# Performance work log

Measured on AMD Instinct MI355X. Metric: run time of the kernel, lower is better.

Reference implementation:

```python
import jax, jax.numpy as jnp
import numpy as np

B, S, D = 2, 2048, 2048
H, DH, DC = 16, 128, 32  # heads, head dim, compressed dim


def setup_inputs() -> dict:
    key = jax.random.key(0)
    ks = jax.random.split(key, 9)
    sc = 0.02
    return {
        "hidden_states": jax.random.normal(ks[0], (B, S, D), jnp.float32),
        "Wq": jax.random.normal(ks[1], (D, D), jnp.float32) * sc,
        "Wk": jax.random.normal(ks[2], (D, D), jnp.float32) * sc,
        "Wv": jax.random.normal(ks[3], (D, D), jnp.float32) * sc,
        "Wo": jax.random.normal(ks[4], (D, D), jnp.float32) * sc,
        "Wkc": jax.random.normal(ks[5], (DH, DC), jnp.float32) * sc,
        "Wvc": jax.random.normal(ks[6], (DH, DC), jnp.float32) * sc,
        "Wke": jax.random.normal(ks[7], (DC, DH), jnp.float32) * sc,
        "Wve": jax.random.normal(ks[8], (DC, DH), jnp.float32) * sc,
    }


def reference(hidden_states, Wq, Wk, Wv, Wo, Wkc, Wvc, Wke, Wve):
    # Project to per-head Q/K/V: [B, H, S, DH]
    def proj(W):
        return jnp.einsum("bsd,de->bse", hidden_states, W).reshape(B, S, H, DH).transpose(0, 2, 1, 3)

    q = proj(Wq)
    k_full = proj(Wk)
    v_full = proj(Wv)

    # Compress K/V (low-rank down-projection, per head): [B, H, S, DC]
    k_compressed = jnp.einsum("bhsd,dc->bhsc", k_full, Wkc)
    v_compressed = jnp.einsum("bhsd,dc->bhsc", v_full, Wvc)

    # Expand compressed cache back to full head dim (expand_mode='pre')
    k_hat = jnp.einsum("bhsc,cd->bhsd", k_compressed, Wke)
    v_hat = jnp.einsum("bhsc,cd->bhsd", v_compressed, Wve)

    # Causal scaled-dot-product attention
    scale = 1.0 / jnp.sqrt(jnp.asarray(DH, jnp.float32))
    scores = jnp.einsum("bhqd,bhkd->bhqk", q, k_hat) * scale
    causal = jnp.tril(jnp.ones((S, S), bool))
    scores = jnp.where(causal[None, None], scores, jnp.finfo(scores.dtype).min)
    probs = jax.nn.softmax(scores, axis=-1)
    ctx = jnp.einsum("bhqk,bhkd->bhqd", probs, v_hat)  # [B, H, S, DH]

    attn_out = jnp.einsum("bsd,de->bse", ctx.transpose(0, 2, 1, 3).reshape(B, S, D), Wo)
    return attn_out, k_compressed, v_compressed
```

## Files before the change

kernel.cpp:

```cpp
#include <hip/hip_runtime.h>

using u16 = unsigned short;
using u32 = unsigned int;

typedef __attribute__((ext_vector_type(8))) __bf16 bf16x8;
typedef __attribute__((ext_vector_type(4))) float f32x4;
typedef __attribute__((ext_vector_type(4))) u32 u32x4;

#define GLOAD16(gp, lp) __builtin_amdgcn_global_load_lds( \
    (const __attribute__((address_space(1))) void*)(gp),  \
    (__attribute__((address_space(3))) void*)(lp), 16, 0, 0)

__device__ __forceinline__ u16 f2b(float f) {
  u32 u = __builtin_bit_cast(u32, f);
  u += 0x7fffu + ((u >> 16) & 1u);
  return (u16)(u >> 16);
}
__device__ __forceinline__ float b2f(u16 h) {
  return __builtin_bit_cast(float, (u32)h << 16);
}

__global__ __launch_bounds__(256) void cast_k(
    const float* __restrict__ in, u16* __restrict__ o1, int n) {
  int i = (blockIdx.x * 256 + threadIdx.x) * 4;
  if (i >= n) return;
  float4 v = *(const float4*)&in[i];
  *(uint2*)&o1[i] = make_uint2((u32)f2b(v.x) | ((u32)f2b(v.y) << 16),
                               (u32)f2b(v.z) | ((u32)f2b(v.w) << 16));
}

__global__ __launch_bounds__(256) void transpose_cast_k(
    const float* __restrict__ in, u16* __restrict__ out, int D) {
  __shared__ float t[32][33];
  const int tx = threadIdx.x & 31, ty = threadIdx.x >> 5;
  const int e0 = blockIdx.x * 32, d0 = blockIdx.y * 32;
  #pragma unroll
  for (int i = ty; i < 32; i += 8) t[i][tx] = in[(size_t)(d0 + i) * D + e0 + tx];
  __syncthreads();
  #pragma unroll
  for (int i = ty; i < 32; i += 8) out[(size_t)(e0 + i) * D + d0 + tx] = f2b(t[tx][i]);
}

__global__ __launch_bounds__(256) void combine_k(
    const float* __restrict__ Wfull, const float* __restrict__ Wc,
    u16* __restrict__ outT, int D) {
  __shared__ float wl[4096];
  const int tid = threadIdx.x;
  for (int i = tid; i < 4096; i += 256) wl[i] = Wc[i];
  __syncthreads();
  const int h = blockIdx.y;
  const int d = blockIdx.x * 256 + tid;
  const float* wkr = Wfull + (size_t)d * D + h * 128;
  float acc[32] = {};
  for (int dp = 0; dp < 128; ++dp) {
    const float wv = wkr[dp];
    const float* w2 = &wl[dp * 32];
    #pragma unroll
    for (int c = 0; c < 32; ++c) acc[c] += wv * w2[c];
  }
  #pragma unroll
  for (int c = 0; c < 32; ++c)
    outT[(size_t)(h * 32 + c) * D + d] = f2b(acc[c]);
}

__global__ __launch_bounds__(256) void wtrans_k(
    const float* __restrict__ in, u16* __restrict__ out) {
  const int i = blockIdx.x * 256 + threadIdx.x;
  const int d = i >> 5, c = i & 31;
  out[i] = f2b(in[c * 128 + d]);
}

template <int TRANS>
__global__ __launch_bounds__(256) void expand_mfma_k(
    const u16* __restrict__ in, const u16* __restrict__ WT, u16* __restrict__ out) {
  __shared__ alignas(16) u16 WL[128 * 32];
  __shared__ alignas(16) u16 ct[64 * 40];
  const int tid = threadIdx.x, lane = tid & 63, w = tid >> 6;
  const int cl = lane & 15, g = lane >> 4;
  const int bh = blockIdx.y, s0 = blockIdx.x * 64;
  for (int i = tid; i < 512; i += 256) ((uint4*)WL)[i] = ((const uint4*)WT)[i];
  {
    const int r = tid >> 2, co = (tid & 3) * 8;
    *(uint4*)&ct[r * 40 + co] =
        *(const uint4*)&in[((size_t)bh * 2048 + s0 + r) * 32 + co];
  }
  __syncthreads();
  f32x4 acc[2][4] = {};
  #pragma unroll
  for (int dti = 0; dti < 2; ++dti) {
    const bf16x8 wf = *(const bf16x8*)&WL[((w * 2 + dti) * 16 + cl) * 32 + g * 8];
    #pragma unroll
    for (int st = 0; st < 4; ++st) {
      const bf16x8 cf = *(const bf16x8*)&ct[(st * 16 + cl) * 40 + g * 8];
      if constexpr (TRANS)
        acc[dti][st] = __builtin_amdgcn_mfma_f32_16x16x32_bf16(wf, cf, acc[dti][st], 0, 0, 0);
      else
        acc[dti][st] = __builtin_amdgcn_mfma_f32_16x16x32_bf16(cf, wf, acc[dti][st], 0, 0, 0);
    }
  }
  #pragma unroll
  for (int dti = 0; dti < 2; ++dti) {
    #pragma unroll
    for (int st = 0; st < 4; ++st) {
      #pragma unroll
      for (int r = 0; r < 4; ++r) {
        if constexpr (TRANS) {
          const int d = (w * 2 + dti) * 16 + g * 4 + r;
          const int s = s0 + st * 16 + cl;
          out[((size_t)bh * 128 + d) * 2048 + s] = f2b(acc[dti][st][r]);
        } else {
          const int s = s0 + st * 16 + g * 4 + r;
          const int d = (w * 2 + dti) * 16 + cl;
          out[((size_t)bh * 2048 + s) * 128 + d] = f2b(acc[dti][st][r]);
        }
      }
    }
  }
}

__global__ __launch_bounds__(256) void gemm_qkv_k(
    const u16* __restrict__ A, const u16* __restrict__ Bt,
    u16* __restrict__ qb, float* __restrict__ out_kc, u16* __restrict__ kcb,
    float* __restrict__ out_vc, u16* __restrict__ vcb) {
  __shared__ alignas(16) u16 As[128 * 64];
  __shared__ alignas(16) u16 Bs[128 * 64];
  const int tid = threadIdx.x, lane = tid & 63, w = tid >> 6;
  const int l15 = lane & 15, lhi = lane >> 4;
  const int m0 = blockIdx.y * 128, n0 = blockIdx.x * 128;
  const int wr = (w >> 1) * 64, wc = (w & 1) * 64;
  const int rl = lane >> 3, cbe = (lane & 7) * 8;
  const int K = 2048;

  f32x4 acc[4][4] = {};

  for (int k0 = 0; k0 < K; k0 += 64) {
    __syncthreads();
    #pragma unroll
    for (int i = 0; i < 4; ++i) {
      const int rb = w * 32 + i * 8;
      GLOAD16(A + (size_t)(m0 + rb + rl) * K + k0 + cbe, &As[rb * 64]);
      GLOAD16(Bt + (size_t)(n0 + rb + rl) * K + k0 + cbe, &Bs[rb * 64]);
    }
    __syncthreads();
    #pragma unroll
    for (int ks = 0; ks < 2; ++ks) {
      bf16x8 af[4], bfr[4];
      #pragma unroll
      for (int m = 0; m < 4; ++m)
        af[m] = *(const bf16x8*)&As[(wr + m * 16 + l15) * 64 + ks * 32 + lhi * 8];
      #pragma unroll
      for (int n = 0; n < 4; ++n)
        bfr[n] = *(const bf16x8*)&Bs[(wc + n * 16 + l15) * 64 + ks * 32 + lhi * 8];
      #pragma unroll
      for (int m = 0; m < 4; ++m)
        #pragma unroll
        for (int n = 0; n < 4; ++n)
          acc[m][n] = __builtin_amdgcn_mfma_f32_16x16x32_bf16(af[m], bfr[n], acc[m][n], 0, 0, 0);
    }
  }

  const float qscale = 0.08838834764831845f;
  #pragma unroll
  for (int m = 0; m < 4; ++m) {
    #pragma unroll
    for (int n = 0; n < 4; ++n) {
      #pragma unroll
      for (int r = 0; r < 4; ++r) {
        const int row = m0 + wr + m * 16 + lhi * 4 + r;
        const int col = n0 + wc + n * 16 + l15;
        const int b = row >> 11, s = row & 2047;
        const float v = acc[m][n][r];
        if (n0 < 2048) {
          const int h = col >> 7, dh = col & 127;
          qb[((size_t)(b * 16 + h) * 2048 + s) * 128 + dh] = f2b(v * qscale);
        } else {
          const int cc = col - 2048;
          if (cc < 512) {
            const int h = cc >> 5, c = cc & 31;
            const size_t idx = ((size_t)(b * 16 + h) * 2048 + s) * 32 + c;
            out_kc[idx] = v;
            kcb[idx] = f2b(v);
          } else {
            const int cc2 = cc - 512;
            const int h = cc2 >> 5, c = cc2 & 31;
            const size_t idx = ((size_t)(b * 16 + h) * 2048 + s) * 32 + c;
            out_vc[idx] = v;
            vcb[idx] = f2b(v);
          }
        }
      }
    }
  }
}

__global__ __launch_bounds__(256) void gemm_o_k(
    const u16* __restrict__ A, const u16* __restrict__ Bt,
    int M, int N, int K, float* __restrict__ outF) {
  __shared__ alignas(16) u16 As[128 * 64];
  __shared__ alignas(16) u16 Bs[128 * 64];
  const int tid = threadIdx.x, lane = tid & 63, w = tid >> 6;
  const int l15 = lane & 15, lhi = lane >> 4;
  const int m0 = blockIdx.y * 128, n0 = blockIdx.x * 128;
  const int wr = (w >> 1) * 64, wc = (w & 1) * 64;
  const int rl = lane >> 3, cbe = (lane & 7) * 8;

  f32x4 acc[4][4] = {};

  for (int k0 = 0; k0 < K; k0 += 64) {
    __syncthreads();
    #pragma unroll
    for (int i = 0; i < 4; ++i) {
      const int rb = w * 32 + i * 8;
      GLOAD16(A + (size_t)(m0 + rb + rl) * K + k0 + cbe, &As[rb * 64]);
      GLOAD16(Bt + (size_t)(n0 + rb + rl) * K + k0 + cbe, &Bs[rb * 64]);
    }
    __syncthreads();
    #pragma unroll
    for (int ks = 0; ks < 2; ++ks) {
      bf16x8 af[4], bfr[4];
      #pragma unroll
      for (int m = 0; m < 4; ++m)
        af[m] = *(const bf16x8*)&As[(wr + m * 16 + l15) * 64 + ks * 32 + lhi * 8];
      #pragma unroll
      for (int n = 0; n < 4; ++n)
        bfr[n] = *(const bf16x8*)&Bs[(wc + n * 16 + l15) * 64 + ks * 32 + lhi * 8];
      #pragma unroll
      for (int m = 0; m < 4; ++m)
        #pragma unroll
        for (int n = 0; n < 4; ++n)
          acc[m][n] = __builtin_amdgcn_mfma_f32_16x16x32_bf16(af[m], bfr[n], acc[m][n], 0, 0, 0);
    }
  }

  #pragma unroll
  for (int m = 0; m < 4; ++m)
    #pragma unroll
    for (int n = 0; n < 4; ++n)
      #pragma unroll
      for (int r = 0; r < 4; ++r)
        outF[(size_t)(m0 + wr + m * 16 + lhi * 4 + r) * N + n0 + wc + n * 16 + l15] =
            acc[m][n][r];
}

__global__ __launch_bounds__(256) void attn_k(
    const u16* __restrict__ q, const u16* __restrict__ kh,
    const u16* __restrict__ vt, u16* __restrict__ ctx) {
  __shared__ alignas(16) u16 Ks[64 * 128];
  __shared__ alignas(16) u16 Vs[128 * 64];
  const int tid = threadIdx.x, lane = tid & 63, w = tid >> 6;
  const int c = lane & 15, g = lane >> 4;
  const int qt = blockIdx.x, bh = blockIdx.y;
  const size_t base = (size_t)bh * (2048 * 128);

  bf16x8 qf[4];
  const int qrow = qt * 64 + w * 16 + c;
  #pragma unroll
  for (int ks = 0; ks < 4; ++ks)
    qf[ks] = *(const bf16x8*)&q[base + (size_t)qrow * 128 + ks * 32 + g * 8];

  f32x4 of[8] = {};
  float m = -__builtin_inff(), l = 0.f;
  const int srcLo = lane ^ (((4 - g) & 3) << 4);
  const int srcHi = lane ^ (((g + 1) & 3) << 4);
  const int alS = (lane & 48) + ((lane & 48) >> 2);
  const bool hiSel = (g >> 1) != 0;

  for (int j = 0; j <= qt; ++j) {
    __syncthreads();
    #pragma unroll
    for (int i = 0; i < 4; ++i) {
      const int rowgrp = w * 16 + i * 4;
      const int rloc = rowgrp + (lane >> 4);
      const int srce = ((c * 16) ^ ((rloc & 7) << 4)) >> 1;
      GLOAD16(kh + base + (size_t)(j * 64 + rloc) * 128 + srce, &Ks[rowgrp * 128]);
    }
    #pragma unroll
    for (int i = 0; i < 4; ++i) {
      const int d0 = (w * 4 + i) * 8;
      const int dd = d0 + (lane >> 3);
      const int cc = lane & 7;
      GLOAD16(vt + base + (size_t)dd * 2048 + j * 64 + ((cc ^ (dd & 7)) * 8),
              &Vs[d0 * 64]);
    }
    __syncthreads();

    f32x4 sf[4] = {};
    #pragma unroll
    for (int n = 0; n < 4; ++n) {
      const int row = n * 16 + c;
      const char* kb = (const char*)Ks + row * 256;
      #pragma unroll
      for (int ks = 0; ks < 4; ++ks) {
        const bf16x8 kf = *(const bf16x8*)(kb + ((ks * 64 + g * 16) ^ ((row & 7) << 4)));
        sf[n] = __builtin_amdgcn_mfma_f32_16x16x32_bf16(kf, qf[ks], sf[n], 0, 0, 0);
      }
    }
    if (j == qt) {
      const int qloc = w * 16 + c;
      #pragma unroll
      for (int n = 0; n < 4; ++n)
        #pragma unroll
        for (int r = 0; r < 4; ++r)
          if (n * 16 + g * 4 + r > qloc) sf[n][r] = -__builtin_inff();
    }
    float smax = sf[0][0];
    #pragma unroll
    for (int n = 0; n < 4; ++n)
      #pragma unroll
      for (int r = 0; r < 4; ++r) smax = fmaxf(smax, sf[n][r]);
    smax = fmaxf(smax, __shfl_xor(smax, 16, 64));
    smax = fmaxf(smax, __shfl_xor(smax, 32, 64));
    if (__any(smax - m > 8.0f)) {
      const float mn = fmaxf(m, smax);
      const float al = __expf(m - mn);
      m = mn;
      l *= al;
      float alr[4];
      #pragma unroll
      for (int r = 0; r < 4; ++r) alr[r] = __shfl(al, alS + r, 64);
      #pragma unroll
      for (int nd = 0; nd < 8; ++nd)
        #pragma unroll
        for (int r = 0; r < 4; ++r) of[nd][r] *= alr[r];
    }
    float rs = 0.f;
    #pragma unroll
    for (int n = 0; n < 4; ++n)
      #pragma unroll
      for (int r = 0; r < 4; ++r) {
        const float p = __expf(sf[n][r] - m);
        sf[n][r] = p;
        rs += p;
      }
    rs += __shfl_xor(rs, 16, 64);
    rs += __shfl_xor(rs, 32, 64);
    l += rs;
    u32 pk0[4], pk1[4];
    #pragma unroll
    for (int n = 0; n < 4; ++n) {
      pk0[n] = (u32)f2b(sf[n][0]) | ((u32)f2b(sf[n][1]) << 16);
      pk1[n] = (u32)f2b(sf[n][2]) | ((u32)f2b(sf[n][3]) << 16);
    }
    bf16x8 pf[2];
    #pragma unroll
    for (int ks2 = 0; ks2 < 2; ++ks2) {
      const int na = ks2 * 2, nb = ks2 * 2 + 1;
      const u32 a0 = (u32)__shfl((int)pk0[na], srcLo, 64);
      const u32 b0 = (u32)__shfl((int)pk0[nb], srcLo, 64);
      const u32 a1 = (u32)__shfl((int)pk1[na], srcLo, 64);
      const u32 b1 = (u32)__shfl((int)pk1[nb], srcLo, 64);
      const u32 a2 = (u32)__shfl((int)pk0[na], srcHi, 64);
      const u32 b2 = (u32)__shfl((int)pk0[nb], srcHi, 64);
      const u32 a3 = (u32)__shfl((int)pk1[na], srcHi, 64);
      const u32 b3 = (u32)__shfl((int)pk1[nb], srcHi, 64);
      const u32x4 wv = {hiSel ? b0 : a0, hiSel ? b1 : a1, hiSel ? b2 : a2, hiSel ? b3 : a3};
      pf[ks2] = __builtin_bit_cast(bf16x8, wv);
    }
    #pragma unroll
    for (int ks2 = 0; ks2 < 2; ++ks2) {
      #pragma unroll
      for (int nd = 0; nd < 8; ++nd) {
        const int row = nd * 16 + c;
        const bf16x8 vf = *(const bf16x8*)((const char*)Vs + row * 128 +
                                           ((ks2 * 64 + g * 16) ^ ((row & 7) << 4)));
        of[nd] = __builtin_amdgcn_mfma_f32_16x16x32_bf16(pf[ks2], vf, of[nd], 0, 0, 0);
      }
    }
  }
  float linv[4];
  #pragma unroll
  for (int r = 0; r < 4; ++r) linv[r] = 1.0f / __shfl(l, alS + r, 64);
  const int bq = bh >> 4, hq = bh & 15;
  #pragma unroll
  for (int nd = 0; nd < 8; ++nd) {
    #pragma unroll
    for (int r = 0; r < 4; ++r) {
      const int row = qt * 64 + w * 16 + g * 4 + r;
      ctx[((size_t)(bq * 2048 + row)) * 2048 + hq * 128 + nd * 16 + c] =
          f2b(of[nd][r] * linv[r]);
    }
  }
}

extern "C" void kernel_launch(void* const* d_in, const int* in_sizes, int n_in,
                              void* d_out, int out_size, void* d_ws, size_t ws_size,
                              hipStream_t stream) {
  const float* hs  = (const float*)d_in[0];
  const float* Wq  = (const float*)d_in[1];
  const float* Wk  = (const float*)d_in[2];
  const float* Wv  = (const float*)d_in[3];
  const float* Wo  = (const float*)d_in[4];
  const float* Wkc = (const float*)d_in[5];
  const float* Wvc = (const float*)d_in[6];
  const float* Wke = (const float*)d_in[7];
  const float* Wve = (const float*)d_in[8];
  float* out      = (float*)d_out;
  float* out_attn = out;
  float* out_kc   = out + 8388608;
  float* out_vc   = out_kc + 2097152;

  char* ws = (char*)d_ws;
  u16* hsb   = (u16*)ws; ws += 16777216;
  u16* BtAll = (u16*)ws; ws += 12582912;
  u16* kcb   = (u16*)ws; ws += 4194304;
  u16* vcb   = (u16*)ws; ws += 4194304;
  u16* WoT   = (u16*)ws; ws += 8388608;
  u16* qb    = (u16*)ws; ws += 16777216;
  u16* vht   = (u16*)ws; ws += 16777216;
  u16* WkeT  = (u16*)ws; ws += 8192;
  u16* WveT  = (u16*)ws; ws += 8192;
  u16* khb   = hsb;
  u16* ctxb  = BtAll;

  cast_k<<<8192, 256, 0, stream>>>(hs, hsb, 8388608);
  transpose_cast_k<<<dim3(64, 64), 256, 0, stream>>>(Wq, BtAll, 2048);
  transpose_cast_k<<<dim3(64, 64), 256, 0, stream>>>(Wo, WoT, 2048);
  combine_k<<<dim3(8, 16), 256, 0, stream>>>(Wk, Wkc, BtAll + (size_t)2048 * 2048, 2048);
  combine_k<<<dim3(8, 16), 256, 0, stream>>>(Wv, Wvc, BtAll + (size_t)2560 * 2048, 2048);
  wtrans_k<<<16, 256, 0, stream>>>(Wke, WkeT);
  wtrans_k<<<16, 256, 0, stream>>>(Wve, WveT);

  gemm_qkv_k<<<dim3(24, 32), 256, 0, stream>>>(hsb, BtAll, qb, out_kc, kcb, out_vc, vcb);

  expand_mfma_k<0><<<dim3(32, 32), 256, 0, stream>>>(kcb, WkeT, khb);
  expand_mfma_k<1><<<dim3(32, 32), 256, 0, stream>>>(vcb, WveT, vht);

  attn_k<<<dim3(32, 32), 256, 0, stream>>>(qb, khb, vht, ctxb);

  gemm_o_k<<<dim3(16, 32), 256, 0, stream>>>(ctxb, WoT, 4096, 2048, 2048, out_attn);
}
```

Before: 494.9 us.

## Pair causal query tiles per block, double-buffer K/V, use exp2 softmax

Each attention block now handles two query tiles (i and 31-i), so every block does the same amount of causal work and the K/V tiles loaded for the longer tile are reused by the shorter one. K/V staging is double-buffered so the next tile's global-to-LDS loads overlap compute, cutting one barrier per iteration. The log2(e) factor is folded into the Q scale so softmax can use exp2f, P is packed to bf16 with the hardware cvt_pk instruction, and the rescale threshold is raised. In exchange the grid is halved to 512 blocks, register and LDS use per block grow, which may lower occupancy.

```diff
diff --git a/kernel.cpp b/kernel.cpp
--- a/kernel.cpp
+++ b/kernel.cpp
@@ -18,6 +18,11 @@
 }
 __device__ __forceinline__ float b2f(u16 h) {
   return __builtin_bit_cast(float, (u32)h << 16);
+}
+__device__ __forceinline__ u32 cvtpk(float lo, float hi) {
+  u32 r;
+  asm("v_cvt_pk_bf16_f32 %0, %1, %2" : "=v"(r) : "v"(lo), "v"(hi));
+  return r;
 }
 
 __global__ __launch_bounds__(256) void cast_k(
@@ -159,7 +164,7 @@
     }
   }
 
-  const float qscale = 0.08838834764831845f;
+  const float qscale = 0.08838834764831845f * 1.4426950408889634f;
   #pragma unroll
   for (int m = 0; m < 4; ++m) {
     #pragma unroll
@@ -245,141 +250,185 @@
 __global__ __launch_bounds__(256) void attn_k(
     const u16* __restrict__ q, const u16* __restrict__ kh,
     const u16* __restrict__ vt, u16* __restrict__ ctx) {
-  __shared__ alignas(16) u16 Ks[64 * 128];
-  __shared__ alignas(16) u16 Vs[128 * 64];
+  __shared__ alignas(16) u16 Ks[2][64 * 128];
+  __shared__ alignas(16) u16 Vs[2][128 * 64];
   const int tid = threadIdx.x, lane = tid & 63, w = tid >> 6;
   const int c = lane & 15, g = lane >> 4;
-  const int qt = blockIdx.x, bh = blockIdx.y;
+  const int iA = blockIdx.x, iB = 31 - iA, bh = blockIdx.y;
   const size_t base = (size_t)bh * (2048 * 128);
 
-  bf16x8 qf[4];
-  const int qrow = qt * 64 + w * 16 + c;
-  #pragma unroll
-  for (int ks = 0; ks < 4; ++ks)
-    qf[ks] = *(const bf16x8*)&q[base + (size_t)qrow * 128 + ks * 32 + g * 8];
-
-  f32x4 of[8] = {};
-  float m = -__builtin_inff(), l = 0.f;
+  bf16x8 qfA[4], qfB[4];
+  {
+    const int qrA = iA * 64 + w * 16 + c;
+    const int qrB = iB * 64 + w * 16 + c;
+    #pragma unroll
+    for (int ks = 0; ks < 4; ++ks) {
+      qfA[ks] = *(const bf16x8*)&q[base + (size_t)qrA * 128 + ks * 32 + g * 8];
+      qfB[ks] = *(const bf16x8*)&q[base + (size_t)qrB * 128 + ks * 32 + g * 8];
+    }
+  }
+
+  f32x4 ofA[8] = {}, ofB[8] = {};
+  float mA = -__builtin_inff(), lA = 0.f;
+  float mB = -__builtin_inff(), lB = 0.f;
   const int srcLo = lane ^ (((4 - g) & 3) << 4);
   const int srcHi = lane ^ (((g + 1) & 3) << 4);
   const int alS = (lane & 48) + ((lane & 48) >> 2);
   const bool hiSel = (g >> 1) != 0;
 
-  for (int j = 0; j <= qt; ++j) {
+#define STAGE(J, BUF)                                                          \
+  {                                                                            \
+    _Pragma("unroll")                                                          \
+    for (int i2 = 0; i2 < 4; ++i2) {                                           \
+      const int rowgrp = w * 16 + i2 * 4;                                      \
+      const int rloc = rowgrp + (lane >> 4);                                   \
+      const int srce = ((c * 16) ^ ((rloc & 7) << 4)) >> 1;                    \
+      GLOAD16(kh + base + (size_t)((J) * 64 + rloc) * 128 + srce,              \
+              &Ks[BUF][rowgrp * 128]);                                         \
+    }                                                                          \
+    _Pragma("unroll")                                                          \
+    for (int i2 = 0; i2 < 4; ++i2) {                                           \
+      const int d0 = (w * 4 + i2) * 8;                                         \
+      const int dd = d0 + (lane >> 3);                                         \
+      const int cc = lane & 7;                                                 \
+      GLOAD16(vt + base + (size_t)dd * 2048 + (J) * 64 + ((cc ^ (dd & 7)) * 8),\
+              &Vs[BUF][d0 * 64]);                                              \
+    }                                                                          \
+  }
+
+#define DO_GROUP(QF, OF, MM, LL, QTILE, J, BUF)                                \
+  {                                                                            \
+    f32x4 sf[4] = {};                                                          \
+    const char* ksb0 = (const char*)&Ks[BUF][0];                               \
+    _Pragma("unroll")                                                          \
+    for (int n = 0; n < 4; ++n) {                                              \
+      const int row = n * 16 + c;                                              \
+      const char* kb = ksb0 + row * 256;                                       \
+      _Pragma("unroll")                                                        \
+      for (int ks = 0; ks < 4; ++ks) {                                         \
+        const bf16x8 kf =                                                      \
+            *(const bf16x8*)(kb + ((ks * 64 + g * 16) ^ ((row & 7) << 4)));    \
+        sf[n] = __builtin_amdgcn_mfma_f32_16x16x32_bf16(kf, QF[ks], sf[n],     \
+                                                        0, 0, 0);              \
+      }                                                                        \
+    }                                                                          \
+    if ((J) == (QTILE)) {                                                      \
+      const int qloc = w * 16 + c;                                             \
+      _Pragma("unroll")                                                        \
+      for (int n = 0; n < 4; ++n)                                              \
+        _Pragma("unroll")                                                      \
+        for (int r = 0; r < 4; ++r)                                            \
+          if (n * 16 + g * 4 + r > qloc) sf[n][r] = -__builtin_inff();         \
+    }                                                                          \
+    float smax = sf[0][0];                                                     \
+    _Pragma("unroll")                                                          \
+    for (int n = 0; n < 4; ++n)                                                \
+      _Pragma("unroll")                                                        \
+      for (int r = 0; r < 4; ++r) smax = fmaxf(smax, sf[n][r]);                \
+    smax = fmaxf(smax, __shfl_xor(smax, 16, 64));                              \
+    smax = fmaxf(smax, __shfl_xor(smax, 32, 64));                              \
+    if (__any(smax - (MM) > 12.0f)) {                                          \
+      const float mn = fmaxf(MM, smax);                                        \
+      const float al = exp2f((MM) - mn);                                       \
+      MM = mn;                                                                 \
+      LL *= al;                                                                \
+      float alr[4];                                                            \
+      _Pragma("unroll")                                                        \
+      for (int r = 0; r < 4; ++r) alr[r] = __shfl(al, alS + r, 64);            \
+      _Pragma("unroll")                                                        \
+      for (int nd = 0; nd < 8; ++nd)                                           \
+        _Pragma("unroll")                                                      \
+        for (int r = 0; r < 4; ++r) OF[nd][r] *= alr[r];                       \
+    }                                                                          \
+    float rs = 0.f;                                                            \
+    _Pragma("unroll")                                                          \
+    for (int n = 0; n < 4; ++n)                                                \
+      _Pragma("unroll")                                                        \
+      for (int r = 0; r < 4; ++r) {                                            \
+        const float p = exp2f(sf[n][r] - (MM));                                \
+        sf[n][r] = p;                                                          \
+        rs += p;                                                               \
+      }                                                                        \
+    rs += __shfl_xor(rs, 16, 64);                                              \
+    rs += __shfl_xor(rs, 32, 64);                                              \
+    LL += rs;                                                                  \
+    u32 pk0[4], pk1[4];                                                        \
+    _Pragma("unroll")                                                          \
+    for (int n = 0; n < 4; ++n) {                                              \
+      pk0[n] = cvtpk(sf[n][0], sf[n][1]);                                      \
+      pk1[n] = cvtpk(sf[n][2], sf[n][3]);                                      \
+    }                                                                          \
+    bf16x8 pf[2];                                                              \
+    _Pragma("unroll")                                                          \
+    for (int ks2 = 0; ks2 < 2; ++ks2) {                                        \
+      const int na = ks2 * 2, nb = ks2 * 2 + 1;                                \
+      const u32 a0 = (u32)__shfl((int)pk0[na], srcLo, 64);                     \
+      const u32 b0 = (u32)__shfl((int)pk0[nb], srcLo, 64);                     \
+      const u32 a1 = (u32)__shfl((int)pk1[na], srcLo, 64);                     \
+      const u32 b1 = (u32)__shfl((int)pk1[nb], srcLo, 64);                     \
+      const u32 a2 = (u32)__shfl((int)pk0[na], srcHi, 64);                     \
+      const u32 b2 = (u32)__shfl((int)pk0[nb], srcHi, 64);                     \
+      const u32 a3 = (u32)__shfl((int)pk1[na], srcHi, 64);                     \
+      const u32 b3 = (u32)__shfl((int)pk1[nb], srcHi, 64);                     \
+      const u32x4 wv = {hiSel ? b0 : a0, hiSel ? b1 : a1, hiSel ? b2 : a2,     \
+                        hiSel ? b3 : a3};                                      \
+      pf[ks2] = __builtin_bit_cast(bf16x8, wv);                                \
+    }                                                                          \
+    const char* vsb0 = (const char*)&Vs[BUF][0];                               \
+    _Pragma("unroll")                                                          \
+    for (int ks2 = 0; ks2 < 2; ++ks2) {                                        \
+      _Pragma("unroll")                                                        \
+      for (int nd = 0; nd < 8; ++nd) {                                         \
+        const int row = nd * 16 + c;                                           \
+        const bf16x8 vf = *(const bf16x8*)(vsb0 + row * 128 +                  \
+            ((ks2 * 64 + g * 16) ^ ((row & 7) << 4)));                         \
+        OF[nd] = __builtin_amdgcn_mfma_f32_16x16x32_bf16(pf[ks2], vf, OF[nd],  \
+                                                         0, 0, 0);             \
+      }                                                                        \
+    }                                                                          \
+  }
+
+  const int jmax = iB;
+  STAGE(0, 0);
+  for (int j = 0; j <= jmax; ++j) {
+    const int buf = j & 1;
     __syncthreads();
-    #pragma unroll
-    for (int i = 0; i < 4; ++i) {
-      const int rowgrp = w * 16 + i * 4;
-      const int rloc = rowgrp + (lane >> 4);
-      const int srce = ((c * 16) ^ ((rloc & 7) << 4)) >> 1;
-      GLOAD16(kh + base + (size_t)(j * 64 + rloc) * 128 + srce, &Ks[rowgrp * 128]);
-    }
-    #pragma unroll
-    for (int i = 0; i < 4; ++i) {
-      const int d0 = (w * 4 + i) * 8;
-      const int dd = d0 + (lane >> 3);
-      const int cc = lane & 7;
-      GLOAD16(vt + base + (size_t)dd * 2048 + j * 64 + ((cc ^ (dd & 7)) * 8),
-              &Vs[d0 * 64]);
-    }
-    __syncthreads();
-
-    f32x4 sf[4] = {};
-    #pragma unroll
-    for (int n = 0; n < 4; ++n) {
-      const int row = n * 16 + c;
-      const char* kb = (const char*)Ks + row * 256;
-      #pragma unroll
-      for (int ks = 0; ks < 4; ++ks) {
-        const bf16x8 kf = *(const bf16x8*)(kb + ((ks * 64 + g * 16) ^ ((row & 7) << 4)));
-        sf[n] = __builtin_amdgcn_mfma_f32_16x16x32_bf16(kf, qf[ks], sf[n], 0, 0, 0);
+    if (j < jmax) STAGE(j + 1, buf ^ 1);
+    if (j <= iA) DO_GROUP(qfA, ofA, mA, lA, iA, j, buf);
+    DO_GROUP(qfB, ofB, mB, lB, iB, j, buf);
+  }
+
+  const int bq = bh >> 4, hq = bh & 15;
+  {
+    float linv[4];
+    #pragma unroll
+    for (int r = 0; r < 4; ++r) linv[r] = 1.0f / __shfl(lA, alS + r, 64);
+    #pragma unroll
+    for (int nd = 0; nd < 8; ++nd) {
+      #pragma unroll
+      for (int r = 0; r < 4; ++r) {
+        const int row = iA * 64 + w * 16 + g * 4 + r;
+        ctx[((size_t)(bq * 2048 + row)) * 2048 + hq * 128 + nd * 16 + c] =
+            f2b(ofA[nd][r] * linv[r]);
       }
     }
-    if (j == qt) {
-      const int qloc = w * 16 + c;
-      #pragma unroll
-      for (int n = 0; n < 4; ++n)
-        #pragma unroll
-        for (int r = 0; r < 4; ++r)
-          if (n * 16 + g * 4 + r > qloc) sf[n][r] = -__builtin_inff();
-    }
-    float smax = sf[0][0];
-    #pragma unroll
-    for (int n = 0; n < 4; ++n)
-      #pragma unroll
-      for (int r = 0; r < 4; ++r) smax = fmaxf(smax, sf[n][r]);
-    smax = fmaxf(smax, __shfl_xor(smax, 16, 64));
-    smax = fmaxf(smax, __shfl_xor(smax, 32, 64));
-    if (__any(smax - m > 8.0f)) {
-      const float mn = fmaxf(m, smax);
-      const float al = __expf(m - mn);
-      m = mn;
-      l *= al;
-      float alr[4];
-      #pragma unroll
-      for (int r = 0; r < 4; ++r) alr[r] = __shfl(al, alS + r, 64);
-      #pragma unroll
-      for (int nd = 0; nd < 8; ++nd)
-        #pragma unroll
-        for (int r = 0; r < 4; ++r) of[nd][r] *= alr[r];
-    }
-    float rs = 0.f;
-    #pragma unroll
-    for (int n = 0; n < 4; ++n)
+  }
+  {
+    float linv[4];
+    #pragma unroll
+    for (int r = 0; r < 4; ++r) linv[r] = 1.0f / __shfl(lB, alS + r, 64);
+    #pragma unroll
+    for (int nd = 0; nd < 8; ++nd) {
       #pragma unroll
       for (int r = 0; r < 4; ++r) {
-        const float p = __expf(sf[n][r] - m);
-        sf[n][r] = p;
-        rs += p;
+        const int row = iB * 64 + w * 16 + g * 4 + r;
+        ctx[((size_t)(bq * 2048 + row)) * 2048 + hq * 128 + nd * 16 + c] =
+            f2b(ofB[nd][r] * linv[r]);
       }
-    rs += __shfl_xor(rs, 16, 64);
-    rs += __shfl_xor(rs, 32, 64);
-    l += rs;
-    u32 pk0[4], pk1[4];
-    #pragma unroll
-    for (int n = 0; n < 4; ++n) {
-      pk0[n] = (u32)f2b(sf[n][0]) | ((u32)f2b(sf[n][1]) << 16);
-      pk1[n] = (u32)f2b(sf[n][2]) | ((u32)f2b(sf[n][3]) << 16);
-    }
-    bf16x8 pf[2];
-    #pragma unroll
-    for (int ks2 = 0; ks2 < 2; ++ks2) {
-      const int na = ks2 * 2, nb = ks2 * 2 + 1;
-      const u32 a0 = (u32)__shfl((int)pk0[na], srcLo, 64);
-      const u32 b0 = (u32)__shfl((int)pk0[nb], srcLo, 64);
-      const u32 a1 = (u32)__shfl((int)pk1[na], srcLo, 64);
-      const u32 b1 = (u32)__shfl((int)pk1[nb], srcLo, 64);
-      const u32 a2 = (u32)__shfl((int)pk0[na], srcHi, 64);
-      const u32 b2 = (u32)__shfl((int)pk0[nb], srcHi, 64);
-      const u32 a3 = (u32)__shfl((int)pk1[na], srcHi, 64);
-      const u32 b3 = (u32)__shfl((int)pk1[nb], srcHi, 64);
-      const u32x4 wv = {hiSel ? b0 : a0, hiSel ? b1 : a1, hiSel ? b2 : a2, hiSel ? b3 : a3};
-      pf[ks2] = __builtin_bit_cast(bf16x8, wv);
-    }
-    #pragma unroll
-    for (int ks2 = 0; ks2 < 2; ++ks2) {
-      #pragma unroll
-      for (int nd = 0; nd < 8; ++nd) {
-        const int row = nd * 16 + c;
-        const bf16x8 vf = *(const bf16x8*)((const char*)Vs + row * 128 +
-                                           ((ks2 * 64 + g * 16) ^ ((row & 7) << 4)));
-        of[nd] = __builtin_amdgcn_mfma_f32_16x16x32_bf16(pf[ks2], vf, of[nd], 0, 0, 0);
-      }
-    }
-  }
-  float linv[4];
-  #pragma unroll
-  for (int r = 0; r < 4; ++r) linv[r] = 1.0f / __shfl(l, alS + r, 64);
-  const int bq = bh >> 4, hq = bh & 15;
-  #pragma unroll
-  for (int nd = 0; nd < 8; ++nd) {
-    #pragma unroll
-    for (int r = 0; r < 4; ++r) {
-      const int row = qt * 64 + w * 16 + g * 4 + r;
-      ctx[((size_t)(bq * 2048 + row)) * 2048 + hq * 128 + nd * 16 + c] =
-          f2b(of[nd][r] * linv[r]);
-    }
-  }
+    }
+  }
+#undef STAGE
+#undef DO_GROUP
 }
 
 extern "C" void kernel_launch(void* const* d_in, const int* in_sizes, int n_in,
@@ -425,7 +474,7 @@
   expand_mfma_k<0><<<dim3(32, 32), 256, 0, stream>>>(kcb, WkeT, khb);
   expand_mfma_k<1><<<dim3(32, 32), 256, 0, stream>>>(vcb, WveT, vht);
 
-  attn_k<<<dim3(32, 32), 256, 0, stream>>>(qb, khb, vht, ctxb);
+  attn_k<<<dim3(16, 32), 256, 0, stream>>>(qb, khb, vht, ctxb);
 
   gemm_o_k<<<dim3(16, 32), 256, 0, stream>>>(ctxb, WoT, 4096, 2048, 2048, out_attn);
 }
```

New measurement: 493.7 us. Within noise of the previous version (-0.2%).

## Pair causal query tiles per block, double-buffer K/V, and use exp2 softmax

Applied to the files above, without the earlier changes.

The attention kernel now runs 512 threads as two 4-wave groups. Each group handles a mirrored query tile (i and 31-i), so every block does about the same causal work and the two groups share the K/V tiles loaded into LDS. K/V loads are double-buffered so the next tile is fetched while the current one is computed, and MFMA sections get raised wave priority. The log2(e) factor is folded into the Q scale so softmax can use exp2, the rescale threshold is loosened to 12, and packing uses the hardware bf16 pack instruction. Doubling LDS and the larger block may limit occupancy.

```diff
diff --git a/kernel.cpp b/kernel.cpp
--- a/kernel.cpp
+++ b/kernel.cpp
@@ -18,6 +18,11 @@
 }
 __device__ __forceinline__ float b2f(u16 h) {
   return __builtin_bit_cast(float, (u32)h << 16);
+}
+__device__ __forceinline__ u32 cvtpk(float lo, float hi) {
+  u32 r;
+  asm("v_cvt_pk_bf16_f32 %0, %1, %2" : "=v"(r) : "v"(lo), "v"(hi));
+  return r;
 }
 
 __global__ __launch_bounds__(256) void cast_k(
@@ -159,7 +164,7 @@
     }
   }
 
-  const float qscale = 0.08838834764831845f;
+  const float qscale = 0.08838834764831845f * 1.4426950408889634f;
   #pragma unroll
   for (int m = 0; m < 4; ++m) {
     #pragma unroll
@@ -242,21 +247,25 @@
             acc[m][n][r];
 }
 
-__global__ __launch_bounds__(256) void attn_k(
+__global__ __launch_bounds__(512, 4) void attn_k(
     const u16* __restrict__ q, const u16* __restrict__ kh,
     const u16* __restrict__ vt, u16* __restrict__ ctx) {
-  __shared__ alignas(16) u16 Ks[64 * 128];
-  __shared__ alignas(16) u16 Vs[128 * 64];
+  __shared__ alignas(16) u16 Ks[2][64 * 128];
+  __shared__ alignas(16) u16 Vs[2][128 * 64];
   const int tid = threadIdx.x, lane = tid & 63, w = tid >> 6;
+  const int grp = w >> 2, wq = w & 3;
   const int c = lane & 15, g = lane >> 4;
-  const int qt = blockIdx.x, bh = blockIdx.y;
+  const int iA = blockIdx.x, iB = 31 - iA, bh = blockIdx.y;
+  const int qt = grp ? iB : iA;
   const size_t base = (size_t)bh * (2048 * 128);
 
   bf16x8 qf[4];
-  const int qrow = qt * 64 + w * 16 + c;
-  #pragma unroll
-  for (int ks = 0; ks < 4; ++ks)
-    qf[ks] = *(const bf16x8*)&q[base + (size_t)qrow * 128 + ks * 32 + g * 8];
+  {
+    const int qrow = qt * 64 + wq * 16 + c;
+    #pragma unroll
+    for (int ks = 0; ks < 4; ++ks)
+      qf[ks] = *(const bf16x8*)&q[base + (size_t)qrow * 128 + ks * 32 + g * 8];
+  }
 
   f32x4 of[8] = {};
   float m = -__builtin_inff(), l = 0.f;
@@ -265,121 +274,141 @@
   const int alS = (lane & 48) + ((lane & 48) >> 2);
   const bool hiSel = (g >> 1) != 0;
 
-  for (int j = 0; j <= qt; ++j) {
+#define STAGE(J, BUF)                                                          \
+  {                                                                            \
+    _Pragma("unroll")                                                          \
+    for (int i2 = 0; i2 < 2; ++i2) {                                           \
+      const int rowgrp = w * 8 + i2 * 4;                                       \
+      const int rloc = rowgrp + (lane >> 4);                                   \
+      const int srce = ((c * 16) ^ ((rloc & 7) << 4)) >> 1;                    \
+      GLOAD16(kh + base + (size_t)((J) * 64 + rloc) * 128 + srce,              \
+              &Ks[BUF][rowgrp * 128]);                                         \
+    }                                                                          \
+    _Pragma("unroll")                                                          \
+    for (int i2 = 0; i2 < 2; ++i2) {                                           \
+      const int d0 = (w * 2 + i2) * 8;                                         \
+      const int dd = d0 + (lane >> 3);                                         \
+      const int cc = lane & 7;                                                 \
+      GLOAD16(vt + base + (size_t)dd * 2048 + (J) * 64 + ((cc ^ (dd & 7)) * 8),\
+              &Vs[BUF][d0 * 64]);                                              \
+    }                                                                          \
+  }
+
+  STAGE(0, 0);
+  for (int j = 0; j <= iB; ++j) {
+    const int buf = j & 1;
     __syncthreads();
-    #pragma unroll
-    for (int i = 0; i < 4; ++i) {
-      const int rowgrp = w * 16 + i * 4;
-      const int rloc = rowgrp + (lane >> 4);
-      const int srce = ((c * 16) ^ ((rloc & 7) << 4)) >> 1;
-      GLOAD16(kh + base + (size_t)(j * 64 + rloc) * 128 + srce, &Ks[rowgrp * 128]);
-    }
-    #pragma unroll
-    for (int i = 0; i < 4; ++i) {
-      const int d0 = (w * 4 + i) * 8;
-      const int dd = d0 + (lane >> 3);
-      const int cc = lane & 7;
-      GLOAD16(vt + base + (size_t)dd * 2048 + j * 64 + ((cc ^ (dd & 7)) * 8),
-              &Vs[d0 * 64]);
-    }
-    __syncthreads();
-
-    f32x4 sf[4] = {};
-    #pragma unroll
-    for (int n = 0; n < 4; ++n) {
-      const int row = n * 16 + c;
-      const char* kb = (const char*)Ks + row * 256;
-      #pragma unroll
-      for (int ks = 0; ks < 4; ++ks) {
-        const bf16x8 kf = *(const bf16x8*)(kb + ((ks * 64 + g * 16) ^ ((row & 7) << 4)));
-        sf[n] = __builtin_amdgcn_mfma_f32_16x16x32_bf16(kf, qf[ks], sf[n], 0, 0, 0);
-      }
-    }
-    if (j == qt) {
-      const int qloc = w * 16 + c;
+    if (j < iB) STAGE(j + 1, buf ^ 1);
+    if (j <= qt) {
+      f32x4 sf[4] = {};
+      const char* ksb0 = (const char*)&Ks[buf][0];
+      __builtin_amdgcn_s_setprio(1);
+      #pragma unroll
+      for (int n = 0; n < 4; ++n) {
+        const int row = n * 16 + c;
+        const char* kb = ksb0 + row * 256;
+        #pragma unroll
+        for (int ks = 0; ks < 4; ++ks) {
+          const bf16x8 kf =
+              *(const bf16x8*)(kb + ((ks * 64 + g * 16) ^ ((row & 7) << 4)));
+          sf[n] = __builtin_amdgcn_mfma_f32_16x16x32_bf16(kf, qf[ks], sf[n], 0, 0, 0);
+        }
+      }
+      __builtin_amdgcn_s_setprio(0);
+      if (j == qt) {
+        const int qloc = wq * 16 + c;
+        #pragma unroll
+        for (int n = 0; n < 4; ++n)
+          #pragma unroll
+          for (int r = 0; r < 4; ++r)
+            if (n * 16 + g * 4 + r > qloc) sf[n][r] = -__builtin_inff();
+      }
+      float smax = sf[0][0];
       #pragma unroll
       for (int n = 0; n < 4; ++n)
         #pragma unroll
-        for (int r = 0; r < 4; ++r)
-          if (n * 16 + g * 4 + r > qloc) sf[n][r] = -__builtin_inff();
-    }
-    float smax = sf[0][0];
-    #pragma unroll
-    for (int n = 0; n < 4; ++n)
-      #pragma unroll
-      for (int r = 0; r < 4; ++r) smax = fmaxf(smax, sf[n][r]);
-    smax = fmaxf(smax, __shfl_xor(smax, 16, 64));
-    smax = fmaxf(smax, __shfl_xor(smax, 32, 64));
-    if (__any(smax - m > 8.0f)) {
-      const float mn = fmaxf(m, smax);
-      const float al = __expf(m - mn);
-      m = mn;
-      l *= al;
-      float alr[4];
-      #pragma unroll
-      for (int r = 0; r < 4; ++r) alr[r] = __shfl(al, alS + r, 64);
-      #pragma unroll
-      for (int nd = 0; nd < 8; ++nd)
-        #pragma unroll
-        for (int r = 0; r < 4; ++r) of[nd][r] *= alr[r];
-    }
-    float rs = 0.f;
-    #pragma unroll
-    for (int n = 0; n < 4; ++n)
+        for (int r = 0; r < 4; ++r) smax = fmaxf(smax, sf[n][r]);
+      smax = fmaxf(smax, __shfl_xor(smax, 16, 64));
+      smax = fmaxf(smax, __shfl_xor(smax, 32, 64));
+      if (__any(smax - m > 12.0f)) {
+        const float mn = fmaxf(m, smax);
+        const float al = exp2f(m - mn);
+        m = mn;
+        l *= al;
+        float alr[4];
+        #pragma unroll
+        for (int r = 0; r < 4; ++r) alr[r] = __shfl(al, alS + r, 64);
+        #pragma unroll
+        for (int nd = 0; nd < 8; ++nd)
+          #pragma unroll
+          for (int r = 0; r < 4; ++r) of[nd][r] *= alr[r];
+      }
+      float rs = 0.f;
+      #pragma unroll
+      for (int n = 0; n < 4; ++n)
+        #pragma unroll
+        for (int r = 0; r < 4; ++r) {
+          const float p = exp2f(sf[n][r] - m);
+          sf[n][r] = p;
+          rs += p;
+        }
+      rs += __shfl_xor(rs, 16, 64);
+      rs += __shfl_xor(rs, 32, 64);
+      l += rs;
+      u32 pk0[4], pk1[4];
+      #pragma unroll
+      for (int n = 0; n < 4; ++n) {
+        pk0[n] = cvtpk(sf[n][0], sf[n][1]);
+        pk1[n] = cvtpk(sf[n][2], sf[n][3]);
+      }
+      bf16x8 pf[2];
+      #pragma unroll
+      for (int ks2 = 0; ks2 < 2; ++ks2) {
+        const int na = ks2 * 2, nb = ks2 * 2 + 1;
+        const u32 a0 = (u32)__shfl((int)pk0[na], srcLo, 64);
+        const u32 b0 = (u32)__shfl((int)pk0[nb], srcLo, 64);
+        const u32 a1 = (u32)__shfl((int)pk1[na], srcLo, 64);
+        const u32 b1 = (u32)__shfl((int)pk1[nb], srcLo, 64);
+        const u32 a2 = (u32)__shfl((int)pk0[na], srcHi, 64);
+        const u32 b2 = (u32)__shfl((int)pk0[nb], srcHi, 64);
+        const u32 a3 = (u32)__shfl((int)pk1[na], srcHi, 64);
+        const u32 b3 = (u32)__shfl((int)pk1[nb], srcHi, 64);
+        const u32x4 wv = {hiSel ? b0 : a0, hiSel ? b1 : a1, hiSel ? b2 : a2,
+                          hiSel ? b3 : a3};
+        pf[ks2] = __builtin_bit_cast(bf16x8, wv);
+      }
+      const char* vsb0 = (const char*)&Vs[buf][0];
+      __builtin_amdgcn_s_setprio(1);
+      #pragma unroll
+      for (int ks2 = 0; ks2 < 2; ++ks2) {
+        #pragma unroll
+        for (int nd = 0; nd < 8; ++nd) {
+          const int row = nd * 16 + c;
+          const bf16x8 vf = *(const bf16x8*)(vsb0 + row * 128 +
+              ((ks2 * 64 + g * 16) ^ ((row & 7) << 4)));
+          of[nd] = __builtin_amdgcn_mfma_f32_16x16x32_bf16(pf[ks2], vf, of[nd], 0, 0, 0);
+        }
+      }
+      __builtin_amdgcn_s_setprio(0);
+    }
+  }
+
+  const int bq = bh >> 4, hq = bh & 15;
+  {
+    float linv[4];
+    #pragma unroll
+    for (int r = 0; r < 4; ++r) linv[r] = 1.0f / __shfl(l, alS + r, 64);
+    #pragma unroll
+    for (int nd = 0; nd < 8; ++nd) {
       #pragma unroll
       for (int r = 0; r < 4; ++r) {
-        const float p = __expf(sf[n][r] - m);
-        sf[n][r] = p;
-        rs += p;
-      }
-    rs += __shfl_xor(rs, 16, 64);
-    rs += __shfl_xor(rs, 32, 64);
-    l += rs;
-    u32 pk0[4], pk1[4];
-    #pragma unroll
-    for (int n = 0; n < 4; ++n) {
-      pk0[n] = (u32)f2b(sf[n][0]) | ((u32)f2b(sf[n][1]) << 16);
-      pk1[n] = (u32)f2b(sf[n][2]) | ((u32)f2b(sf[n][3]) << 16);
-    }
-    bf16x8 pf[2];
-    #pragma unroll
-    for (int ks2 = 0; ks2 < 2; ++ks2) {
-      const int na = ks2 * 2, nb = ks2 * 2 + 1;
-      const u32 a0 = (u32)__shfl((int)pk0[na], srcLo, 64);
-      const u32 b0 = (u32)__shfl((int)pk0[nb], srcLo, 64);
-      const u32 a1 = (u32)__shfl((int)pk1[na], srcLo, 64);
-      const u32 b1 = (u32)__shfl((int)pk1[nb], srcLo, 64);
-      const u32 a2 = (u32)__shfl((int)pk0[na], srcHi, 64);
-      const u32 b2 = (u32)__shfl((int)pk0[nb], srcHi, 64);
-      const u32 a3 = (u32)__shfl((int)pk1[na], srcHi, 64);
-      const u32 b3 = (u32)__shfl((int)pk1[nb], srcHi, 64);
-      const u32x4 wv = {hiSel ? b0 : a0, hiSel ? b1 : a1, hiSel ? b2 : a2, hiSel ? b3 : a3};
-      pf[ks2] = __builtin_bit_cast(bf16x8, wv);
-    }
-    #pragma unroll
-    for (int ks2 = 0; ks2 < 2; ++ks2) {
-      #pragma unroll
-      for (int nd = 0; nd < 8; ++nd) {
-        const int row = nd * 16 + c;
-        const bf16x8 vf = *(const bf16x8*)((const char*)Vs + row * 128 +
-                                           ((ks2 * 64 + g * 16) ^ ((row & 7) << 4)));
-        of[nd] = __builtin_amdgcn_mfma_f32_16x16x32_bf16(pf[ks2], vf, of[nd], 0, 0, 0);
-      }
-    }
-  }
-  float linv[4];
-  #pragma unroll
-  for (int r = 0; r < 4; ++r) linv[r] = 1.0f / __shfl(l, alS + r, 64);
-  const int bq = bh >> 4, hq = bh & 15;
-  #pragma unroll
-  for (int nd = 0; nd < 8; ++nd) {
-    #pragma unroll
-    for (int r = 0; r < 4; ++r) {
-      const int row = qt * 64 + w * 16 + g * 4 + r;
-      ctx[((size_t)(bq * 2048 + row)) * 2048 + hq * 128 + nd * 16 + c] =
-          f2b(of[nd][r] * linv[r]);
-    }
-  }
+        const int row = qt * 64 + wq * 16 + g * 4 + r;
+        ctx[((size_t)(bq * 2048 + row)) * 2048 + hq * 128 + nd * 16 + c] =
+            f2b(of[nd][r] * linv[r]);
+      }
+    }
+  }
+#undef STAGE
 }
 
 extern "C" void kernel_launch(void* const* d_in, const int* in_sizes, int n_in,
@@ -425,7 +454,7 @@
   expand_mfma_k<0><<<dim3(32, 32), 256, 0, stream>>>(kcb, WkeT, khb);
   expand_mfma_k<1><<<dim3(32, 32), 256, 0, stream>>>(vcb, WveT, vht);
 
-  attn_k<<<dim3(32, 32), 256, 0, stream>>>(qb, khb, vht, ctxb);
+  attn_k<<<dim3(16, 32), 512, 0, stream>>>(qb, khb, vht, ctxb);
 
   gemm_o_k<<<dim3(16, 32), 256, 0, stream>>>(ctxb, WoT, 4096, 2048, 2048, out_attn);
 }
```

New measurement: 442.9 us. 1.12x faster.
